# Optimization experiments

Measured on AMD Instinct MI355X. Metric: run time of the kernel, lower is better.

Reference implementation:

```python
import jax, jax.numpy as jnp
import numpy as np

EPS = 1e-5
HEADS = 8


def _bn(x, p):
    # p: [4, C] rows = (gamma, beta, running_mean, running_var); channel axis = 1 (eval-mode BN)
    shape = (1, p.shape[1]) + (1,) * (x.ndim - 2)
    g = p[0].reshape(shape); b = p[1].reshape(shape)
    m = p[2].reshape(shape); v = p[3].reshape(shape)
    return (x - m) * (g / jnp.sqrt(v + EPS)) + b


def _conv1x1(x, w):
    # x: [N, Cin, H, W], w: [Cout, Cin]
    return jnp.einsum('oc,nchw->nohw', w, x)


def _axial(x, kqv_w, kqv_bn, logits_bn, rel_enc, ks, height_dim):
    # x: [B, C, H, W]
    if height_dim:
        x = jnp.transpose(x, (0, 3, 1, 2))  # [B, W, C, H] -> attend over H (=ks)
    else:
        x = jnp.transpose(x, (0, 2, 1, 3))  # [B, H, C, W] -> attend over W (=ks)
    b, w, d, h = x.shape
    dh = d // HEADS
    xf = x.reshape(b * w, d, h)
    kqv = jnp.einsum('oc,ncl->nol', kqv_w, xf)          # conv1d k=1, [n, 2d, h]
    kqv = _bn(kqv, kqv_bn)
    kqv = kqv.reshape(b * w, HEADS, dh * 2, h)
    k = kqv[:, :, : dh // 2]                            # [n, H, dh/2, h]
    q = kqv[:, :, dh // 2: dh]                          # [n, H, dh/2, h]
    v = kqv[:, :, dh:]                                  # [n, H, dh,   h]
    # relative position encodings
    idx = jnp.arange(ks)[None, :] - jnp.arange(ks)[:, None] + ks - 1  # [ks, ks]
    rel = rel_enc[:, idx.reshape(-1)].reshape(dh * 2, ks, ks)
    q_enc = rel[: dh // 2]
    k_enc = rel[dh // 2: dh]
    v_enc = rel[dh:]
    qk = jnp.einsum('nhdx,nhdy->nhxy', q, k)
    qr = jnp.einsum('nhdx,dxy->nhxy', q, q_enc)
    kr = jnp.einsum('nhdx,dxy->nhyx', k, k_enc)         # einsum + transpose(2,3)
    logits = jnp.concatenate([qk, qr, kr], axis=1)       # [n, 3*H, h, h]
    logits = _bn(logits, logits_bn)
    logits = logits.reshape(b * w, 3, HEADS, h, h).sum(axis=1)
    weights = jax.nn.softmax(logits, axis=3)             # [n, H, h, h]
    attn = jnp.einsum('nhxy,nhdy->nhdx', weights, v)
    attn_enc = jnp.einsum('nhxy,dxy->nhdx', weights, v_enc)
    # cat along last dim + reshape + sum(dim=-2) in torch == elementwise sum here
    out = (attn + attn_enc).reshape(b, w, d, h)
    if height_dim:
        out = jnp.transpose(out, (0, 2, 3, 1))  # [B, C, H, W]
    else:
        out = jnp.transpose(out, (0, 2, 1, 3))  # [B, C, H, W]
    return out


def setup_inputs() -> dict:
    key = jax.random.key(0)
    ks = jax.random.split(key, 13)
    def rn(k, shape, s=0.05):
        return jax.random.normal(k, shape, jnp.float32) * s
    def rp(k, shape):
        return jax.random.uniform(k, shape, jnp.float32, minval=0.1, maxval=1.0)
    return {
        'x': jax.random.normal(ks[0], (1, 64, 256, 128), jnp.float32),
        'conv1_w': rn(ks[1], (64, 64)),
        'bn1': rp(ks[2], (4, 64)),
        'kqv_w_h': rn(ks[3], (128, 64)),
        'kqv_bn_h': rp(ks[4], (4, 128)),
        'logits_bn_h': rp(ks[5], (4, 24)),
        'rel_enc_h': rn(ks[6], (16, 511)),
        'kqv_w_w': rn(ks[7], (128, 64)),
        'kqv_bn_w': rp(ks[8], (4, 128)),
        'logits_bn_w': rp(ks[9], (4, 24)),
        'rel_enc_w': rn(ks[10], (16, 255)),
        'conv3_w': rn(ks[11], (64, 64)),
        'bn3': rp(ks[12], (4, 64)),
    }


def reference(x, conv1_w, bn1, kqv_w_h, kqv_bn_h, logits_bn_h, rel_enc_h,
              kqv_w_w, kqv_bn_w, logits_bn_w, rel_enc_w, conv3_w, bn3):
    out = jax.nn.relu(_bn(_conv1x1(x, conv1_w), bn1))
    out = _axial(out, kqv_w_h, kqv_bn_h, logits_bn_h, rel_enc_h, 256, True)
    out = _axial(out, kqv_w_w, kqv_bn_w, logits_bn_w, rel_enc_w, 128, False)
    out = jax.nn.relu(out)
    out = _bn(_conv1x1(out, conv3_w), bn3)
    return jax.nn.relu(out + x)
```

## Files before the change

kernel.cpp:

```cpp
#include <hip/hip_runtime.h>
#include <stdint.h>

#define EPSF 1e-5f
#define LOG2E 1.4426950408889634f

typedef float f32x2 __attribute__((ext_vector_type(2)));
typedef float f32x4 __attribute__((ext_vector_type(4)));

__device__ __forceinline__ float bflo(uint32_t u){ union{uint32_t u;float f;}c; c.u=u<<16; return c.f; }
__device__ __forceinline__ float bfhi(uint32_t u){ union{uint32_t u;float f;}c; c.u=u&0xffff0000u; return c.f; }
__device__ __forceinline__ float bfhiraw(uint32_t u){ union{uint32_t u;float f;}c; c.u=u; return c.f; }
__device__ __forceinline__ uint32_t f2bf(float f){ union{float f;uint32_t u;}c; c.f=f; uint32_t u=c.u; return (u + 0x7fffu + ((u>>16)&1u)) >> 16; }
__device__ __forceinline__ uint32_t pk2(float a, float b){ return f2bf(a) | (f2bf(b)<<16); }

__device__ __forceinline__ f32x2 pk_add(f32x2 a, f32x2 b){
  f32x2 d; asm("v_pk_add_f32 %0, %1, %2" : "=v"(d) : "v"(a), "v"(b)); return d;
}
__device__ __forceinline__ f32x2 pk_mul(f32x2 a, f32x2 b){
  f32x2 d; asm("v_pk_mul_f32 %0, %1, %2" : "=v"(d) : "v"(a), "v"(b)); return d;
}
__device__ __forceinline__ f32x2 pk_fma(f32x2 a, f32x2 b, f32x2 c){
  f32x2 d; asm("v_pk_fma_f32 %0, %1, %2, %3" : "=v"(d) : "v"(a), "v"(b), "v"(c)); return d;
}
__device__ __forceinline__ f32x2 up2(uint32_t u){
  f32x2 r; r.x = bflo(u); r.y = bfhiraw(u); return r;
}

__global__ __launch_bounds__(256)
void k_conv1(const float* __restrict__ in, const float* __restrict__ w,
             const float* __restrict__ bn, float* __restrict__ out,
             const float* __restrict__ relH, const float* __restrict__ relW,
             uint4* __restrict__ rqkH, uint4* __restrict__ rveH,
             uint4* __restrict__ rqkW, uint4* __restrict__ rveW) {
  if (blockIdx.x >= 512) {
    int which = blockIdx.x - 512;
    int NJ = which ? 255 : 511;
    const float* rel = which ? relW : relH;
    uint4* rqk = which ? rqkW : rqkH;
    uint4* rve = which ? rveW : rveH;
    const float* q = rel;
    const float* k = rel + 4*NJ;
    const float* v = rel + 8*NJ;
    for (int j = threadIdx.x; j < NJ; j += 256) {
      int jr = NJ-1-j;
      uint4 a;
      a.x = pk2(q[0*NJ+j], q[1*NJ+j]);
      a.y = pk2(q[2*NJ+j], q[3*NJ+j]);
      a.z = pk2(k[0*NJ+jr], k[1*NJ+jr]);
      a.w = pk2(k[2*NJ+jr], k[3*NJ+jr]);
      rqk[j] = a;
      uint4 b;
      b.x = pk2(v[0*NJ+j], v[1*NJ+j]);
      b.y = pk2(v[2*NJ+j], v[3*NJ+j]);
      b.z = pk2(v[4*NJ+j], v[5*NJ+j]);
      b.w = pk2(v[6*NJ+j], v[7*NJ+j]);
      rve[j] = b;
    }
    return;
  }
  __shared__ float L[64*65];
  int tid = threadIdx.x;
  int p0 = blockIdx.x * 64;
  int lane = tid & 63;
  int wvs = __builtin_amdgcn_readfirstlane(tid >> 6);
  #pragma unroll
  for (int rr = 0; rr < 16; ++rr) {
    int c = wvs*16 + rr;
    L[lane*65 + c] = in[(size_t)c*32768 + p0 + lane];
  }
  __syncthreads();
  f32x2 xv2[32];
  #pragma unroll
  for (int c2 = 0; c2 < 32; ++c2) {
    xv2[c2].x = L[lane*65 + 2*c2];
    xv2[c2].y = L[lane*65 + 2*c2 + 1];
  }
  float val[16];
  #pragma unroll
  for (int r = 0; r < 16; ++r) {
    int o = wvs*16 + r;
    const f32x2* wr = (const f32x2*)(w + o*64);
    f32x2 a2 = {0.f, 0.f};
    #pragma unroll
    for (int c2 = 0; c2 < 32; ++c2) a2 = wr[c2]*xv2[c2] + a2;
    float acc = a2.x + a2.y;
    float s = bn[o] * rsqrtf(bn[192+o] + EPSF);
    val[r] = fmaxf(fmaf(acc, s, fmaf(-bn[128+o], s, bn[64+o])), 0.f);
  }
  __syncthreads();
  #pragma unroll
  for (int r = 0; r < 16; ++r) L[lane*65 + wvs*16 + r] = val[r];
  __syncthreads();
  float4* dst = (float4*)(out + (size_t)p0*64);
  #pragma unroll
  for (int k = 0; k < 4; ++k) {
    int f4 = tid + k*256;
    int f = f4*4; int p = f >> 6, o = f & 63;
    float4 v;
    v.x = L[p*65+o]; v.y = L[p*65+o+1]; v.z = L[p*65+o+2]; v.w = L[p*65+o+3];
    dst[f4] = v;
  }
}

template<int LEN, int RS, int CS>
__global__ __launch_bounds__(512)
void k_kqv(const float* __restrict__ in, const float* __restrict__ w,
           const float* __restrict__ bn, uint4* __restrict__ kvV,
           uint2* __restrict__ kvK, float* __restrict__ qb) {
  __shared__ float L[64*65];
  int tid = threadIdx.x;
  int n = blockIdx.x;
  int y0 = blockIdx.y * 64;
  #pragma unroll
  for (int rr = 0; rr < 8; ++rr) {
    int idx = tid + rr*512;
    int yy = idx >> 6, c = idx & 63;
    L[yy*65 + c] = in[((size_t)(y0+yy)*RS + (size_t)n*CS)*64 + c];
  }
  __syncthreads();
  int hd = __builtin_amdgcn_readfirstlane(tid >> 6);
  int yy = tid & 63;
  f32x2 xv2[32];
  #pragma unroll
  for (int c2 = 0; c2 < 32; ++c2) {
    xv2[c2].x = L[yy*65 + 2*c2];
    xv2[c2].y = L[yy*65 + 2*c2 + 1];
  }
  float val[16];
  #pragma unroll
  for (int r = 0; r < 16; ++r) {
    int o = hd*16 + r;
    const f32x2* wr = (const f32x2*)(w + o*64);
    f32x2 a2 = {0.f, 0.f};
    #pragma unroll
    for (int c2 = 0; c2 < 32; ++c2) a2 = wr[c2]*xv2[c2] + a2;
    float acc = a2.x + a2.y;
    float s = bn[o] * rsqrtf(bn[384+o] + EPSF);
    val[r] = fmaf(acc, s, fmaf(-bn[256+o], s, bn[128+o]));
  }
  size_t base = ((size_t)n*8 + hd)*LEN + (y0 + yy);
  kvK[base] = make_uint2(pk2(val[0],val[1]), pk2(val[2],val[3]));
  kvV[base] = make_uint4(pk2(val[8],val[9]),  pk2(val[10],val[11]),
                         pk2(val[12],val[13]), pk2(val[14],val[15]));
  float4 qq; qq.x = val[4]; qq.y = val[5]; qq.z = val[6]; qq.w = val[7];
  *(float4*)(qb + base*4) = qq;
}

struct E4 { f32x2 qe0, qe1, ke0, ke1; };
struct V4 { f32x2 a, b, c, d; };

__device__ __forceinline__ E4 upQK(uint4 u){
  E4 r; r.qe0 = up2(u.x); r.qe1 = up2(u.y); r.ke0 = up2(u.z); r.ke1 = up2(u.w); return r;
}
__device__ __forceinline__ V4 upVE(uint4 u){
  V4 r; r.a = up2(u.x); r.b = up2(u.y); r.c = up2(u.z); r.d = up2(u.w); return r;
}
__device__ __forceinline__ float pairA(f32x2 q01, f32x2 q23, const E4& e,
                                       f32x2 ktlo, f32x2 kthi) {
  f32x2 t0 = pk_add(q01, e.ke0);
  f32x2 t1 = pk_add(q23, e.ke1);
  f32x2 s  = pk_mul(t0, ktlo);
  s = pk_fma(t1, kthi, s);
  s = pk_fma(q01, e.qe0, s);
  s = pk_fma(q23, e.qe1, s);
  return s.x + s.y;
}
__device__ __forceinline__ void pairB(float ex, const V4& ve,
                                      f32x2 va01, f32x2 va23, f32x2 vb01, f32x2 vb23,
                                      f32x2* A, float& ss) {
  ss += ex;
  f32x2 e2; e2.x = ex; e2.y = ex;
  A[0] = pk_fma(e2, pk_add(va01, ve.a), A[0]);
  A[1] = pk_fma(e2, pk_add(va23, ve.b), A[1]);
  A[2] = pk_fma(e2, pk_add(vb01, ve.c), A[2]);
  A[3] = pk_fma(e2, pk_add(vb23, ve.d), A[3]);
}

template<int LEN, int NB, int G, bool RELUO, int XS, int NS>
__device__ __forceinline__
void attn_body(const uint4* __restrict__ kvV, const uint2* __restrict__ kvK,
               const float* __restrict__ qb, const uint4* __restrict__ rqk,
               const uint4* __restrict__ rve, const float* __restrict__ lbn,
               float* __restrict__ out) {
  constexpr int NJ = 2*LEN-1;
  constexpr int NJ4 = (NJ+1)/4;
  constexpr int XT = LEN/4;
  constexpr int T = NB*XT*G;
  constexpr int YR = LEN/G;
  constexpr size_t S1 = (size_t)NB*LEN*48 + (size_t)NJ4*4*16*2;
  constexpr size_t S2 = (size_t)(G-1)*NB*LEN*40;
  constexpr size_t PS = S1 > S2 ? S1 : S2;
  int nb = blockIdx.x >> 3;
  int hd = blockIdx.x & 7;
  int n0 = nb * NB;
  int t  = threadIdx.x;

  __shared__ __align__(16) char pool[PS];
  f32x4* sKt = (f32x4*)(pool);
  f32x4* sVa = (f32x4*)(pool + (size_t)NB*LEN*16);
  f32x4* sVb = (f32x4*)(pool + (size_t)NB*LEN*32);
  uint4* tQK = (uint4*)(pool + (size_t)NB*LEN*48);
  uint4* tVE = (uint4*)(pool + (size_t)NB*LEN*48 + (size_t)NJ4*64);

  float A0L, A1L, A2L;
  {
    int c0 = hd, c1 = 8+hd, c2 = 16+hd;
    A0L = lbn[c0]*rsqrtf(lbn[72+c0]+EPSF)*LOG2E;
    A1L = lbn[c1]*rsqrtf(lbn[72+c1]+EPSF)*LOG2E;
    A2L = lbn[c2]*rsqrtf(lbn[72+c2]+EPSF)*LOG2E;
  }
  float A0g = (fabsf(A0L) > 1e-25f) ? A0L : copysignf(1e-25f, A0L);
  float ratio = A2L / A0g;

  for (int i = t; i < NB*LEN; i += T) {
    int nn = i / LEN, yy = i % LEN;
    size_t src = ((size_t)(n0+nn)*8 + hd)*LEN + yy;
    uint2 kk = kvK[src];
    uint4 vv = kvV[src];
    f32x4 kt; kt.x=bflo(kk.x)*A0g; kt.y=bfhi(kk.x)*A0g; kt.z=bflo(kk.y)*A0g; kt.w=bfhi(kk.y)*A0g;
    sKt[i] = kt;
    f32x4 va; va.x=bflo(vv.x); va.y=bfhi(vv.x); va.z=bflo(vv.y); va.w=bfhi(vv.y);
    sVa[i] = va;
    f32x4 vb; vb.x=bflo(vv.z); vb.y=bfhi(vv.z); vb.z=bflo(vv.w); vb.w=bfhi(vv.w);
    sVb[i] = vb;
  }
  for (int j = t; j < NJ; j += T) {
    uint4 a = rqk[j];
    uint4 sq;
    sq.x = pk2(bflo(a.x)*A1L,   bfhi(a.x)*A1L);
    sq.y = pk2(bflo(a.y)*A1L,   bfhi(a.y)*A1L);
    sq.z = pk2(bflo(a.z)*ratio, bfhi(a.z)*ratio);
    sq.w = pk2(bflo(a.w)*ratio, bfhi(a.w)*ratio);
    int r = j & 3, mm = j >> 2;
    tQK[r*NJ4 + mm] = sq;
    tVE[r*NJ4 + mm] = rve[j];
  }

  int g  = t / (NB*XT);
  int u  = t % (NB*XT);
  int ni = u / XT;
  int tl = u % XT;
  int y0 = g * YR;
  int x0 = 4 * tl;
  int niL = ni * LEN;
  size_t kb = ((size_t)(n0+ni)*8 + hd)*LEN;

  f32x2 q01[4], q23[4];
  #pragma unroll
  for (int i = 0; i < 4; ++i) {
    f32x4 qq = *(const f32x4*)(qb + (kb + x0 + i)*4);
    q01[i].x = qq.x; q01[i].y = qq.y;
    q23[i].x = qq.z; q23[i].y = qq.w;
  }

  float m[4], ss[4];
  f32x2 acc[4][4];
  #pragma unroll
  for (int i=0;i<4;++i){ m[i]=-3.0e38f; ss[i]=0.f;
    #pragma unroll
    for(int d=0;d<4;++d){ acc[i][d].x=0.f; acc[i][d].y=0.f; } }

  __syncthreads();

  int mi = ((y0 + LEN-1) >> 2) - (x0 >> 2);
  E4 Wq0 = upQK(tQK[0*NJ4 + mi]), Wq1 = upQK(tQK[1*NJ4 + mi]), Wq2 = upQK(tQK[2*NJ4 + mi]);
  V4 Wv0 = upVE(tVE[0*NJ4 + mi]), Wv1 = upVE(tVE[1*NJ4 + mi]), Wv2 = upVE(tVE[2*NJ4 + mi]);

  for (int cc = 0; cc < YR/4; ++cc) {
    int yb = niL + y0 + 4*cc;
    int ma = mi + cc;
    int mb = ma + 1;
    float lr[4][4];
    E4 E3 = upQK(tQK[3*NJ4 + ma]);
    { f32x4 kt = sKt[yb]; f32x2 kl = kt.lo, kh = kt.hi;
      lr[0][0]=pairA(q01[0],q23[0],E3, kl,kh); lr[1][0]=pairA(q01[1],q23[1],Wq2,kl,kh);
      lr[2][0]=pairA(q01[2],q23[2],Wq1,kl,kh); lr[3][0]=pairA(q01[3],q23[3],Wq0,kl,kh); }
    E4 E0 = upQK(tQK[0*NJ4 + mb]);
    { f32x4 kt = sKt[yb+1]; f32x2 kl = kt.lo, kh = kt.hi;
      lr[0][1]=pairA(q01[0],q23[0],E0, kl,kh); lr[1][1]=pairA(q01[1],q23[1],E3, kl,kh);
      lr[2][1]=pairA(q01[2],q23[2],Wq2,kl,kh); lr[3][1]=pairA(q01[3],q23[3],Wq1,kl,kh); }
    E4 E1 = upQK(tQK[1*NJ4 + mb]);
    { f32x4 kt = sKt[yb+2]; f32x2 kl = kt.lo, kh = kt.hi;
      lr[0][2]=pairA(q01[0],q23[0],E1, kl,kh); lr[1][2]=pairA(q01[1],q23[1],E0, kl,kh);
      lr[2][2]=pairA(q01[2],q23[2],E3, kl,kh); lr[3][2]=pairA(q01[3],q23[3],Wq2,kl,kh); }
    E4 E2 = upQK(tQK[2*NJ4 + mb]);
    { f32x4 kt = sKt[yb+3]; f32x2 kl = kt.lo, kh = kt.hi;
      lr[0][3]=pairA(q01[0],q23[0],E2, kl,kh); lr[1][3]=pairA(q01[1],q23[1],E1, kl,kh);
      lr[2][3]=pairA(q01[2],q23[2],E0, kl,kh); lr[3][3]=pairA(q01[3],q23[3],E3, kl,kh); }
    Wq0 = E0; Wq1 = E1; Wq2 = E2;
    float cm[4];
    bool need = false;
    #pragma unroll
    for (int i = 0; i < 4; ++i) {
      cm[i] = fmaxf(fmaxf(lr[i][0], lr[i][1]), fmaxf(lr[i][2], lr[i][3]));
      need = need || (cm[i] > m[i]);
    }
    if (__any(need)) {
      #pragma unroll
      for (int i = 0; i < 4; ++i) {
        float mn = fmaxf(m[i], cm[i]);
        float sc = __builtin_amdgcn_exp2f(m[i] - mn);
        m[i] = mn; ss[i] *= sc;
        f32x2 sc2; sc2.x = sc; sc2.y = sc;
        #pragma unroll
        for (int d = 0; d < 4; ++d) acc[i][d] = pk_mul(acc[i][d], sc2);
      }
    }
    V4 F3 = upVE(tVE[3*NJ4 + ma]);
    { f32x4 va = sVa[yb], vb = sVb[yb];
      pairB(__builtin_amdgcn_exp2f(lr[0][0]-m[0]), F3,  va.lo,va.hi,vb.lo,vb.hi, acc[0], ss[0]);
      pairB(__builtin_amdgcn_exp2f(lr[1][0]-m[1]), Wv2, va.lo,va.hi,vb.lo,vb.hi, acc[1], ss[1]);
      pairB(__builtin_amdgcn_exp2f(lr[2][0]-m[2]), Wv1, va.lo,va.hi,vb.lo,vb.hi, acc[2], ss[2]);
      pairB(__builtin_amdgcn_exp2f(lr[3][0]-m[3]), Wv0, va.lo,va.hi,vb.lo,vb.hi, acc[3], ss[3]); }
    V4 F0 = upVE(tVE[0*NJ4 + mb]);
    { f32x4 va = sVa[yb+1], vb = sVb[yb+1];
      pairB(__builtin_amdgcn_exp2f(lr[0][1]-m[0]), F0,  va.lo,va.hi,vb.lo,vb.hi, acc[0], ss[0]);
      pairB(__builtin_amdgcn_exp2f(lr[1][1]-m[1]), F3,  va.lo,va.hi,vb.lo,vb.hi, acc[1], ss[1]);
      pairB(__builtin_amdgcn_exp2f(lr[2][1]-m[2]), Wv2, va.lo,va.hi,vb.lo,vb.hi, acc[2], ss[2]);
      pairB(__builtin_amdgcn_exp2f(lr[3][1]-m[3]), Wv1, va.lo,va.hi,vb.lo,vb.hi, acc[3], ss[3]); }
    V4 F1 = upVE(tVE[1*NJ4 + mb]);
    { f32x4 va = sVa[yb+2], vb = sVb[yb+2];
      pairB(__builtin_amdgcn_exp2f(lr[0][2]-m[0]), F1,  va.lo,va.hi,vb.lo,vb.hi, acc[0], ss[0]);
      pairB(__builtin_amdgcn_exp2f(lr[1][2]-m[1]), F0,  va.lo,va.hi,vb.lo,vb.hi, acc[1], ss[1]);
      pairB(__builtin_amdgcn_exp2f(lr[2][2]-m[2]), F3,  va.lo,va.hi,vb.lo,vb.hi, acc[2], ss[2]);
      pairB(__builtin_amdgcn_exp2f(lr[3][2]-m[3]), Wv2, va.lo,va.hi,vb.lo,vb.hi, acc[3], ss[3]); }
    V4 F2 = upVE(tVE[2*NJ4 + mb]);
    { f32x4 va = sVa[yb+3], vb = sVb[yb+3];
      pairB(__builtin_amdgcn_exp2f(lr[0][3]-m[0]), F2,  va.lo,va.hi,vb.lo,vb.hi, acc[0], ss[0]);
      pairB(__builtin_amdgcn_exp2f(lr[1][3]-m[1]), F1,  va.lo,va.hi,vb.lo,vb.hi, acc[1], ss[1]);
      pairB(__builtin_amdgcn_exp2f(lr[2][3]-m[2]), F0,  va.lo,va.hi,vb.lo,vb.hi, acc[2], ss[2]);
      pairB(__builtin_amdgcn_exp2f(lr[3][3]-m[3]), F3,  va.lo,va.hi,vb.lo,vb.hi, acc[3], ss[3]); }
    Wv0 = F0; Wv1 = F1; Wv2 = F2;
  }

  __syncthreads();
  float4* M0 = (float4*)(pool);
  float4* M1 = (float4*)(pool + (size_t)(G-1)*NB*LEN*16);
  float2* MS = (float2*)(pool + (size_t)(G-1)*NB*LEN*32);
  int xb = niL + x0;
  if (g > 0) {
    #pragma unroll
    for (int i = 0; i < 4; ++i) {
      int slot = (g-1)*NB*LEN + xb + i;
      M0[slot] = make_float4(acc[i][0].x,acc[i][0].y,acc[i][1].x,acc[i][1].y);
      M1[slot] = make_float4(acc[i][2].x,acc[i][2].y,acc[i][3].x,acc[i][3].y);
      MS[slot] = make_float2(m[i], ss[i]);
    }
  }
  __syncthreads();
  if (g == 0) {
    #pragma unroll
    for (int i = 0; i < 4; ++i) {
      float M = m[i];
      float2 oms[G-1];
      #pragma unroll
      for (int gg = 1; gg < G; ++gg) {
        oms[gg-1] = MS[(gg-1)*NB*LEN + xb + i];
        M = fmaxf(M, oms[gg-1].x);
      }
      float w0 = __builtin_amdgcn_exp2f(m[i] - M);
      float st = ss[i]*w0;
      float a[8];
      a[0]=acc[i][0].x*w0; a[1]=acc[i][0].y*w0; a[2]=acc[i][1].x*w0; a[3]=acc[i][1].y*w0;
      a[4]=acc[i][2].x*w0; a[5]=acc[i][2].y*w0; a[6]=acc[i][3].x*w0; a[7]=acc[i][3].y*w0;
      #pragma unroll
      for (int gg = 1; gg < G; ++gg) {
        int slot = (gg-1)*NB*LEN + xb + i;
        float wg = __builtin_amdgcn_exp2f(oms[gg-1].x - M);
        st += oms[gg-1].y*wg;
        float4 a0 = M0[slot];
        float4 a1 = M1[slot];
        a[0] = fmaf(a0.x, wg, a[0]); a[1] = fmaf(a0.y, wg, a[1]);
        a[2] = fmaf(a0.z, wg, a[2]); a[3] = fmaf(a0.w, wg, a[3]);
        a[4] = fmaf(a1.x, wg, a[4]); a[5] = fmaf(a1.y, wg, a[5]);
        a[6] = fmaf(a1.z, wg, a[6]); a[7] = fmaf(a1.w, wg, a[7]);
      }
      float inv = 1.0f / st;
      float* dst = out + ((size_t)(x0+i)*XS + (size_t)(n0+ni)*NS)*64 + hd*8;
      float4 lo, hi;
      lo.x = a[0]*inv; lo.y = a[1]*inv; lo.z = a[2]*inv; lo.w = a[3]*inv;
      hi.x = a[4]*inv; hi.y = a[5]*inv; hi.z = a[6]*inv; hi.w = a[7]*inv;
      if (RELUO) {
        lo.x=fmaxf(lo.x,0.f); lo.y=fmaxf(lo.y,0.f); lo.z=fmaxf(lo.z,0.f); lo.w=fmaxf(lo.w,0.f);
        hi.x=fmaxf(hi.x,0.f); hi.y=fmaxf(hi.y,0.f); hi.z=fmaxf(hi.z,0.f); hi.w=fmaxf(hi.w,0.f);
      }
      *(float4*)dst = lo;
      *((float4*)dst + 1) = hi;
    }
  }
}

__global__ __launch_bounds__(256, 2)
void k_attnH(const uint4* __restrict__ kvV, const uint2* __restrict__ kvK,
             const float* __restrict__ qb, const uint4* __restrict__ rqk,
             const uint4* __restrict__ rve, const float* __restrict__ lbn,
             float* __restrict__ out) {
  attn_body<256,1,4,false,128,1>(kvV, kvK, qb, rqk, rve, lbn, out);
}
__global__ __launch_bounds__(256, 2)
void k_attnW(const uint4* __restrict__ kvV, const uint2* __restrict__ kvK,
             const float* __restrict__ qb, const uint4* __restrict__ rqk,
             const uint4* __restrict__ rve, const float* __restrict__ lbn,
             float* __restrict__ out) {
  attn_body<128,2,4,true,1,128>(kvV, kvK, qb, rqk, rve, lbn, out);
}

__global__ __launch_bounds__(256)
void k_conv3(const float* __restrict__ in, const float* __restrict__ w,
             const float* __restrict__ bn, const float* __restrict__ resid,
             float* __restrict__ out) {
  __shared__ float L[64*65];
  int tid = threadIdx.x;
  int p0 = blockIdx.x * 64;
  const float4* src = (const float4*)(in + (size_t)p0*64);
  #pragma unroll
  for (int k = 0; k < 4; ++k) {
    int f4 = tid + k*256;
    float4 v = src[f4];
    int f = f4*4; int p = f >> 6, o = f & 63;
    L[p*65+o] = v.x; L[p*65+o+1] = v.y; L[p*65+o+2] = v.z; L[p*65+o+3] = v.w;
  }
  __syncthreads();
  int lane = tid & 63;
  int wvs = __builtin_amdgcn_readfirstlane(tid >> 6);
  f32x2 xv2[32];
  #pragma unroll
  for (int c2 = 0; c2 < 32; ++c2) {
    xv2[c2].x = L[lane*65 + 2*c2];
    xv2[c2].y = L[lane*65 + 2*c2 + 1];
  }
  #pragma unroll
  for (int r = 0; r < 16; ++r) {
    int o = wvs*16 + r;
    const f32x2* wr = (const f32x2*)(w + o*64);
    f32x2 a2 = {0.f, 0.f};
    #pragma unroll
    for (int c2 = 0; c2 < 32; ++c2) a2 = wr[c2]*xv2[c2] + a2;
    float acc = a2.x + a2.y;
    float s = bn[o] * rsqrtf(bn[192+o] + EPSF);
    float val = fmaf(acc, s, fmaf(-bn[128+o], s, bn[64+o]));
    size_t idx = (size_t)o*32768 + p0 + lane;
    out[idx] = fmaxf(val + resid[idx], 0.f);
  }
}

extern "C" void kernel_launch(void* const* d_in, const int* in_sizes, int n_in,
                              void* d_out, int out_size, void* d_ws, size_t ws_size,
                              hipStream_t stream) {
  const float* x         = (const float*)d_in[0];
  const float* conv1_w   = (const float*)d_in[1];
  const float* bn1       = (const float*)d_in[2];
  const float* kqv_w_h   = (const float*)d_in[3];
  const float* kqv_bn_h  = (const float*)d_in[4];
  const float* lbn_h     = (const float*)d_in[5];
  const float* rel_h     = (const float*)d_in[6];
  const float* kqv_w_w   = (const float*)d_in[7];
  const float* kqv_bn_w  = (const float*)d_in[8];
  const float* lbn_w     = (const float*)d_in[9];
  const float* rel_w     = (const float*)d_in[10];
  const float* conv3_w   = (const float*)d_in[11];
  const float* bn3       = (const float*)d_in[12];
  float* outp = (float*)d_out;
  char* ws = (char*)d_ws;

  float* A    = (float*)(ws);
  uint4* kvV  = (uint4*)(ws + 8388608);
  uint2* kvK  = (uint2*)(ws + 12582912);
  float* qb   = (float*)(ws + 14680064);
  uint4* rqkH = (uint4*)(ws + 18874368);
  uint4* rveH = (uint4*)(ws + 18882560);
  uint4* rqkW = (uint4*)(ws + 18890752);
  uint4* rveW = (uint4*)(ws + 18894848);

  k_conv1<<<514, 256, 0, stream>>>(x, conv1_w, bn1, A,
                                   rel_h, rel_w, rqkH, rveH, rqkW, rveW);

  k_kqv<256,128,1><<<dim3(128,4), 512, 0, stream>>>(A, kqv_w_h, kqv_bn_h, kvV, kvK, qb);
  k_attnH<<<1024, 256, 0, stream>>>(kvV, kvK, qb, rqkH, rveH, lbn_h, A);

  k_kqv<128,1,128><<<dim3(256,2), 512, 0, stream>>>(A, kqv_w_w, kqv_bn_w, kvV, kvK, qb);
  k_attnW<<<1024, 256, 0, stream>>>(kvV, kvK, qb, rqkW, rveW, lbn_w, A);

  k_conv3<<<512, 256, 0, stream>>>(A, conv3_w, bn3, x, outp);
}
```

Before: 171.5 us.

## Switch attention operands from bf16 to fp16 with packed dot2 and half-width LDS

Intermediate K, V and relative-encoding tables are now stored as fp16 instead of bf16. The attention inner loop computes logits with fdot2 on packed halves and adds V to V-encodings with packed fp16 adds, instead of unpacking to fp32 and using v_pk_fma. K and V now stay packed in shared memory, which halves that LDS footprint and the load traffic. The aim is fewer ALU instructions per logit and per accumulation, traded for fp16 range and rounding risk and more scalar fp16-to-fp32 converts in the PV accumulation.

```diff
diff --git a/kernel.cpp b/kernel.cpp
--- a/kernel.cpp
+++ b/kernel.cpp
@@ -6,25 +6,26 @@
 
 typedef float f32x2 __attribute__((ext_vector_type(2)));
 typedef float f32x4 __attribute__((ext_vector_type(4)));
-
-__device__ __forceinline__ float bflo(uint32_t u){ union{uint32_t u;float f;}c; c.u=u<<16; return c.f; }
-__device__ __forceinline__ float bfhi(uint32_t u){ union{uint32_t u;float f;}c; c.u=u&0xffff0000u; return c.f; }
-__device__ __forceinline__ float bfhiraw(uint32_t u){ union{uint32_t u;float f;}c; c.u=u; return c.f; }
-__device__ __forceinline__ uint32_t f2bf(float f){ union{float f;uint32_t u;}c; c.f=f; uint32_t u=c.u; return (u + 0x7fffu + ((u>>16)&1u)) >> 16; }
-__device__ __forceinline__ uint32_t pk2(float a, float b){ return f2bf(a) | (f2bf(b)<<16); }
-
-__device__ __forceinline__ f32x2 pk_add(f32x2 a, f32x2 b){
-  f32x2 d; asm("v_pk_add_f32 %0, %1, %2" : "=v"(d) : "v"(a), "v"(b)); return d;
-}
-__device__ __forceinline__ f32x2 pk_mul(f32x2 a, f32x2 b){
-  f32x2 d; asm("v_pk_mul_f32 %0, %1, %2" : "=v"(d) : "v"(a), "v"(b)); return d;
-}
-__device__ __forceinline__ f32x2 pk_fma(f32x2 a, f32x2 b, f32x2 c){
-  f32x2 d; asm("v_pk_fma_f32 %0, %1, %2, %3" : "=v"(d) : "v"(a), "v"(b), "v"(c)); return d;
-}
-__device__ __forceinline__ f32x2 up2(uint32_t u){
-  f32x2 r; r.x = bflo(u); r.y = bfhiraw(u); return r;
-}
+typedef _Float16 h2 __attribute__((ext_vector_type(2)));
+union UH2 { uint32_t u; h2 h; };
+
+__device__ __forceinline__ uint32_t pkh(float a, float b){
+  UH2 c; c.h.x = (_Float16)a; c.h.y = (_Float16)b; return c.u;
+}
+__device__ __forceinline__ h2 ash2(uint32_t u){ UH2 c; c.u = u; return c.h; }
+__device__ __forceinline__ uint32_t padd16(uint32_t a, uint32_t b){
+  UH2 c; c.h = ash2(a) + ash2(b); return c.u;
+}
+#if __has_builtin(__builtin_amdgcn_fdot2)
+__device__ __forceinline__ float fdot2u(uint32_t a, uint32_t b, float c){
+  return __builtin_amdgcn_fdot2(ash2(a), ash2(b), c, false);
+}
+#else
+__device__ __forceinline__ float fdot2u(uint32_t a, uint32_t b, float c){
+  h2 x = ash2(a), y = ash2(b);
+  return fmaf((float)x.y, (float)y.y, fmaf((float)x.x, (float)y.x, c));
+}
+#endif
 
 __global__ __launch_bounds__(256)
 void k_conv1(const float* __restrict__ in, const float* __restrict__ w,
@@ -44,16 +45,16 @@
     for (int j = threadIdx.x; j < NJ; j += 256) {
       int jr = NJ-1-j;
       uint4 a;
-      a.x = pk2(q[0*NJ+j], q[1*NJ+j]);
-      a.y = pk2(q[2*NJ+j], q[3*NJ+j]);
-      a.z = pk2(k[0*NJ+jr], k[1*NJ+jr]);
-      a.w = pk2(k[2*NJ+jr], k[3*NJ+jr]);
+      a.x = pkh(q[0*NJ+j], q[1*NJ+j]);
+      a.y = pkh(q[2*NJ+j], q[3*NJ+j]);
+      a.z = pkh(k[0*NJ+jr], k[1*NJ+jr]);
+      a.w = pkh(k[2*NJ+jr], k[3*NJ+jr]);
       rqk[j] = a;
       uint4 b;
-      b.x = pk2(v[0*NJ+j], v[1*NJ+j]);
-      b.y = pk2(v[2*NJ+j], v[3*NJ+j]);
-      b.z = pk2(v[4*NJ+j], v[5*NJ+j]);
-      b.w = pk2(v[6*NJ+j], v[7*NJ+j]);
+      b.x = pkh(v[0*NJ+j], v[1*NJ+j]);
+      b.y = pkh(v[2*NJ+j], v[3*NJ+j]);
+      b.z = pkh(v[4*NJ+j], v[5*NJ+j]);
+      b.w = pkh(v[6*NJ+j], v[7*NJ+j]);
       rve[j] = b;
     }
     return;
@@ -139,41 +140,34 @@
     val[r] = fmaf(acc, s, fmaf(-bn[256+o], s, bn[128+o]));
   }
   size_t base = ((size_t)n*8 + hd)*LEN + (y0 + yy);
-  kvK[base] = make_uint2(pk2(val[0],val[1]), pk2(val[2],val[3]));
-  kvV[base] = make_uint4(pk2(val[8],val[9]),  pk2(val[10],val[11]),
-                         pk2(val[12],val[13]), pk2(val[14],val[15]));
+  kvK[base] = make_uint2(pkh(val[0],val[1]), pkh(val[2],val[3]));
+  kvV[base] = make_uint4(pkh(val[8],val[9]),  pkh(val[10],val[11]),
+                         pkh(val[12],val[13]), pkh(val[14],val[15]));
   float4 qq; qq.x = val[4]; qq.y = val[5]; qq.z = val[6]; qq.w = val[7];
   *(float4*)(qb + base*4) = qq;
 }
 
-struct E4 { f32x2 qe0, qe1, ke0, ke1; };
-struct V4 { f32x2 a, b, c, d; };
-
-__device__ __forceinline__ E4 upQK(uint4 u){
-  E4 r; r.qe0 = up2(u.x); r.qe1 = up2(u.y); r.ke0 = up2(u.z); r.ke1 = up2(u.w); return r;
-}
-__device__ __forceinline__ V4 upVE(uint4 u){
-  V4 r; r.a = up2(u.x); r.b = up2(u.y); r.c = up2(u.z); r.d = up2(u.w); return r;
-}
-__device__ __forceinline__ float pairA(f32x2 q01, f32x2 q23, const E4& e,
-                                       f32x2 ktlo, f32x2 kthi) {
-  f32x2 t0 = pk_add(q01, e.ke0);
-  f32x2 t1 = pk_add(q23, e.ke1);
-  f32x2 s  = pk_mul(t0, ktlo);
-  s = pk_fma(t1, kthi, s);
-  s = pk_fma(q01, e.qe0, s);
-  s = pk_fma(q23, e.qe1, s);
-  return s.x + s.y;
-}
-__device__ __forceinline__ void pairB(float ex, const V4& ve,
-                                      f32x2 va01, f32x2 va23, f32x2 vb01, f32x2 vb23,
-                                      f32x2* A, float& ss) {
-  ss += ex;
-  f32x2 e2; e2.x = ex; e2.y = ex;
-  A[0] = pk_fma(e2, pk_add(va01, ve.a), A[0]);
-  A[1] = pk_fma(e2, pk_add(va23, ve.b), A[1]);
-  A[2] = pk_fma(e2, pk_add(vb01, ve.c), A[2]);
-  A[3] = pk_fma(e2, pk_add(vb23, ve.d), A[3]);
+__device__ __forceinline__ float pairA(uint32_t q01, uint32_t q23, uint4 e,
+                                       uint32_t kt01, uint32_t kt23) {
+  uint32_t t01 = padd16(q01, e.z);
+  uint32_t t23 = padd16(q23, e.w);
+  return fdot2u(kt01, t01, fdot2u(kt23, t23, fdot2u(q01, e.x, fdot2u(q23, e.y, 0.f))));
+}
+__device__ __forceinline__ void pairB(float e, uint4 ve, uint4 vv,
+                                      float* A, float& ss) {
+  ss += e;
+  h2 w0 = ash2(vv.x) + ash2(ve.x);
+  h2 w1 = ash2(vv.y) + ash2(ve.y);
+  h2 w2 = ash2(vv.z) + ash2(ve.z);
+  h2 w3 = ash2(vv.w) + ash2(ve.w);
+  A[0] = fmaf((float)w0.x, e, A[0]);
+  A[1] = fmaf((float)w0.y, e, A[1]);
+  A[2] = fmaf((float)w1.x, e, A[2]);
+  A[3] = fmaf((float)w1.y, e, A[3]);
+  A[4] = fmaf((float)w2.x, e, A[4]);
+  A[5] = fmaf((float)w2.y, e, A[5]);
+  A[6] = fmaf((float)w3.x, e, A[6]);
+  A[7] = fmaf((float)w3.y, e, A[7]);
 }
 
 template<int LEN, int NB, int G, bool RELUO, int XS, int NS>
@@ -187,7 +181,7 @@
   constexpr int XT = LEN/4;
   constexpr int T = NB*XT*G;
   constexpr int YR = LEN/G;
-  constexpr size_t S1 = (size_t)NB*LEN*48 + (size_t)NJ4*4*16*2;
+  constexpr size_t S1 = (size_t)NB*LEN*24 + (size_t)NJ4*4*16*2;
   constexpr size_t S2 = (size_t)(G-1)*NB*LEN*40;
   constexpr size_t PS = S1 > S2 ? S1 : S2;
   int nb = blockIdx.x >> 3;
@@ -196,11 +190,10 @@
   int t  = threadIdx.x;
 
   __shared__ __align__(16) char pool[PS];
-  f32x4* sKt = (f32x4*)(pool);
-  f32x4* sVa = (f32x4*)(pool + (size_t)NB*LEN*16);
-  f32x4* sVb = (f32x4*)(pool + (size_t)NB*LEN*32);
-  uint4* tQK = (uint4*)(pool + (size_t)NB*LEN*48);
-  uint4* tVE = (uint4*)(pool + (size_t)NB*LEN*48 + (size_t)NJ4*64);
+  uint2* sKt = (uint2*)(pool);
+  uint4* sV2 = (uint4*)(pool + (size_t)NB*LEN*8);
+  uint4* tQK = (uint4*)(pool + (size_t)NB*LEN*24);
+  uint4* tVE = (uint4*)(pool + (size_t)NB*LEN*24 + (size_t)NJ4*64);
 
   float A0L, A1L, A2L;
   {
@@ -216,21 +209,19 @@
     int nn = i / LEN, yy = i % LEN;
     size_t src = ((size_t)(n0+nn)*8 + hd)*LEN + yy;
     uint2 kk = kvK[src];
-    uint4 vv = kvV[src];
-    f32x4 kt; kt.x=bflo(kk.x)*A0g; kt.y=bfhi(kk.x)*A0g; kt.z=bflo(kk.y)*A0g; kt.w=bfhi(kk.y)*A0g;
-    sKt[i] = kt;
-    f32x4 va; va.x=bflo(vv.x); va.y=bfhi(vv.x); va.z=bflo(vv.y); va.w=bfhi(vv.y);
-    sVa[i] = va;
-    f32x4 vb; vb.x=bflo(vv.z); vb.y=bfhi(vv.z); vb.z=bflo(vv.w); vb.w=bfhi(vv.w);
-    sVb[i] = vb;
+    h2 a = ash2(kk.x), b = ash2(kk.y);
+    sKt[i] = make_uint2(pkh(A0g*(float)a.x, A0g*(float)a.y),
+                        pkh(A0g*(float)b.x, A0g*(float)b.y));
+    sV2[i] = kvV[src];
   }
   for (int j = t; j < NJ; j += T) {
     uint4 a = rqk[j];
+    h2 q01 = ash2(a.x), q23 = ash2(a.y), k01 = ash2(a.z), k23 = ash2(a.w);
     uint4 sq;
-    sq.x = pk2(bflo(a.x)*A1L,   bfhi(a.x)*A1L);
-    sq.y = pk2(bflo(a.y)*A1L,   bfhi(a.y)*A1L);
-    sq.z = pk2(bflo(a.z)*ratio, bfhi(a.z)*ratio);
-    sq.w = pk2(bflo(a.w)*ratio, bfhi(a.w)*ratio);
+    sq.x = pkh(A1L*(float)q01.x,   A1L*(float)q01.y);
+    sq.y = pkh(A1L*(float)q23.x,   A1L*(float)q23.y);
+    sq.z = pkh(ratio*(float)k01.x, ratio*(float)k01.y);
+    sq.w = pkh(ratio*(float)k23.x, ratio*(float)k23.y);
     int r = j & 3, mm = j >> 2;
     tQK[r*NJ4 + mm] = sq;
     tVE[r*NJ4 + mm] = rve[j];
@@ -245,48 +236,47 @@
   int niL = ni * LEN;
   size_t kb = ((size_t)(n0+ni)*8 + hd)*LEN;
 
-  f32x2 q01[4], q23[4];
+  uint32_t q01[4], q23[4];
   #pragma unroll
   for (int i = 0; i < 4; ++i) {
     f32x4 qq = *(const f32x4*)(qb + (kb + x0 + i)*4);
-    q01[i].x = qq.x; q01[i].y = qq.y;
-    q23[i].x = qq.z; q23[i].y = qq.w;
-  }
-
-  float m[4], ss[4];
-  f32x2 acc[4][4];
+    q01[i] = pkh(qq.x, qq.y);
+    q23[i] = pkh(qq.z, qq.w);
+  }
+
+  float m[4], ss[4], acc[4][8];
   #pragma unroll
   for (int i=0;i<4;++i){ m[i]=-3.0e38f; ss[i]=0.f;
     #pragma unroll
-    for(int d=0;d<4;++d){ acc[i][d].x=0.f; acc[i][d].y=0.f; } }
+    for(int d=0;d<8;++d) acc[i][d]=0.f; }
 
   __syncthreads();
 
   int mi = ((y0 + LEN-1) >> 2) - (x0 >> 2);
-  E4 Wq0 = upQK(tQK[0*NJ4 + mi]), Wq1 = upQK(tQK[1*NJ4 + mi]), Wq2 = upQK(tQK[2*NJ4 + mi]);
-  V4 Wv0 = upVE(tVE[0*NJ4 + mi]), Wv1 = upVE(tVE[1*NJ4 + mi]), Wv2 = upVE(tVE[2*NJ4 + mi]);
+  uint4 Wq0 = tQK[0*NJ4 + mi], Wq1 = tQK[1*NJ4 + mi], Wq2 = tQK[2*NJ4 + mi];
+  uint4 Wv0 = tVE[0*NJ4 + mi], Wv1 = tVE[1*NJ4 + mi], Wv2 = tVE[2*NJ4 + mi];
 
   for (int cc = 0; cc < YR/4; ++cc) {
     int yb = niL + y0 + 4*cc;
     int ma = mi + cc;
     int mb = ma + 1;
     float lr[4][4];
-    E4 E3 = upQK(tQK[3*NJ4 + ma]);
-    { f32x4 kt = sKt[yb]; f32x2 kl = kt.lo, kh = kt.hi;
-      lr[0][0]=pairA(q01[0],q23[0],E3, kl,kh); lr[1][0]=pairA(q01[1],q23[1],Wq2,kl,kh);
-      lr[2][0]=pairA(q01[2],q23[2],Wq1,kl,kh); lr[3][0]=pairA(q01[3],q23[3],Wq0,kl,kh); }
-    E4 E0 = upQK(tQK[0*NJ4 + mb]);
-    { f32x4 kt = sKt[yb+1]; f32x2 kl = kt.lo, kh = kt.hi;
-      lr[0][1]=pairA(q01[0],q23[0],E0, kl,kh); lr[1][1]=pairA(q01[1],q23[1],E3, kl,kh);
-      lr[2][1]=pairA(q01[2],q23[2],Wq2,kl,kh); lr[3][1]=pairA(q01[3],q23[3],Wq1,kl,kh); }
-    E4 E1 = upQK(tQK[1*NJ4 + mb]);
-    { f32x4 kt = sKt[yb+2]; f32x2 kl = kt.lo, kh = kt.hi;
-      lr[0][2]=pairA(q01[0],q23[0],E1, kl,kh); lr[1][2]=pairA(q01[1],q23[1],E0, kl,kh);
-      lr[2][2]=pairA(q01[2],q23[2],E3, kl,kh); lr[3][2]=pairA(q01[3],q23[3],Wq2,kl,kh); }
-    E4 E2 = upQK(tQK[2*NJ4 + mb]);
-    { f32x4 kt = sKt[yb+3]; f32x2 kl = kt.lo, kh = kt.hi;
-      lr[0][3]=pairA(q01[0],q23[0],E2, kl,kh); lr[1][3]=pairA(q01[1],q23[1],E1, kl,kh);
-      lr[2][3]=pairA(q01[2],q23[2],E0, kl,kh); lr[3][3]=pairA(q01[3],q23[3],E3, kl,kh); }
+    uint4 E3 = tQK[3*NJ4 + ma];
+    { uint2 kt = sKt[yb];
+      lr[0][0]=pairA(q01[0],q23[0],E3, kt.x,kt.y); lr[1][0]=pairA(q01[1],q23[1],Wq2,kt.x,kt.y);
+      lr[2][0]=pairA(q01[2],q23[2],Wq1,kt.x,kt.y); lr[3][0]=pairA(q01[3],q23[3],Wq0,kt.x,kt.y); }
+    uint4 E0 = tQK[0*NJ4 + mb];
+    { uint2 kt = sKt[yb+1];
+      lr[0][1]=pairA(q01[0],q23[0],E0, kt.x,kt.y); lr[1][1]=pairA(q01[1],q23[1],E3, kt.x,kt.y);
+      lr[2][1]=pairA(q01[2],q23[2],Wq2,kt.x,kt.y); lr[3][1]=pairA(q01[3],q23[3],Wq1,kt.x,kt.y); }
+    uint4 E1 = tQK[1*NJ4 + mb];
+    { uint2 kt = sKt[yb+2];
+      lr[0][2]=pairA(q01[0],q23[0],E1, kt.x,kt.y); lr[1][2]=pairA(q01[1],q23[1],E0, kt.x,kt.y);
+      lr[2][2]=pairA(q01[2],q23[2],E3, kt.x,kt.y); lr[3][2]=pairA(q01[3],q23[3],Wq2,kt.x,kt.y); }
+    uint4 E2 = tQK[2*NJ4 + mb];
+    { uint2 kt = sKt[yb+3];
+      lr[0][3]=pairA(q01[0],q23[0],E2, kt.x,kt.y); lr[1][3]=pairA(q01[1],q23[1],E1, kt.x,kt.y);
+      lr[2][3]=pairA(q01[2],q23[2],E0, kt.x,kt.y); lr[3][3]=pairA(q01[3],q23[3],E3, kt.x,kt.y); }
     Wq0 = E0; Wq1 = E1; Wq2 = E2;
     float cm[4];
     bool need = false;
@@ -301,35 +291,34 @@
         float mn = fmaxf(m[i], cm[i]);
         float sc = __builtin_amdgcn_exp2f(m[i] - mn);
         m[i] = mn; ss[i] *= sc;
-        f32x2 sc2; sc2.x = sc; sc2.y = sc;
         #pragma unroll
-        for (int d = 0; d < 4; ++d) acc[i][d] = pk_mul(acc[i][d], sc2);
+        for (int d = 0; d < 8; ++d) acc[i][d] *= sc;
       }
     }
-    V4 F3 = upVE(tVE[3*NJ4 + ma]);
-    { f32x4 va = sVa[yb], vb = sVb[yb];
-      pairB(__builtin_amdgcn_exp2f(lr[0][0]-m[0]), F3,  va.lo,va.hi,vb.lo,vb.hi, acc[0], ss[0]);
-      pairB(__builtin_amdgcn_exp2f(lr[1][0]-m[1]), Wv2, va.lo,va.hi,vb.lo,vb.hi, acc[1], ss[1]);
-      pairB(__builtin_amdgcn_exp2f(lr[2][0]-m[2]), Wv1, va.lo,va.hi,vb.lo,vb.hi, acc[2], ss[2]);
-      pairB(__builtin_amdgcn_exp2f(lr[3][0]-m[3]), Wv0, va.lo,va.hi,vb.lo,vb.hi, acc[3], ss[3]); }
-    V4 F0 = upVE(tVE[0*NJ4 + mb]);
-    { f32x4 va = sVa[yb+1], vb = sVb[yb+1];
-      pairB(__builtin_amdgcn_exp2f(lr[0][1]-m[0]), F0,  va.lo,va.hi,vb.lo,vb.hi, acc[0], ss[0]);
-      pairB(__builtin_amdgcn_exp2f(lr[1][1]-m[1]), F3,  va.lo,va.hi,vb.lo,vb.hi, acc[1], ss[1]);
-      pairB(__builtin_amdgcn_exp2f(lr[2][1]-m[2]), Wv2, va.lo,va.hi,vb.lo,vb.hi, acc[2], ss[2]);
-      pairB(__builtin_amdgcn_exp2f(lr[3][1]-m[3]), Wv1, va.lo,va.hi,vb.lo,vb.hi, acc[3], ss[3]); }
-    V4 F1 = upVE(tVE[1*NJ4 + mb]);
-    { f32x4 va = sVa[yb+2], vb = sVb[yb+2];
-      pairB(__builtin_amdgcn_exp2f(lr[0][2]-m[0]), F1,  va.lo,va.hi,vb.lo,vb.hi, acc[0], ss[0]);
-      pairB(__builtin_amdgcn_exp2f(lr[1][2]-m[1]), F0,  va.lo,va.hi,vb.lo,vb.hi, acc[1], ss[1]);
-      pairB(__builtin_amdgcn_exp2f(lr[2][2]-m[2]), F3,  va.lo,va.hi,vb.lo,vb.hi, acc[2], ss[2]);
-      pairB(__builtin_amdgcn_exp2f(lr[3][2]-m[3]), Wv2, va.lo,va.hi,vb.lo,vb.hi, acc[3], ss[3]); }
-    V4 F2 = upVE(tVE[2*NJ4 + mb]);
-    { f32x4 va = sVa[yb+3], vb = sVb[yb+3];
-      pairB(__builtin_amdgcn_exp2f(lr[0][3]-m[0]), F2,  va.lo,va.hi,vb.lo,vb.hi, acc[0], ss[0]);
-      pairB(__builtin_amdgcn_exp2f(lr[1][3]-m[1]), F1,  va.lo,va.hi,vb.lo,vb.hi, acc[1], ss[1]);
-      pairB(__builtin_amdgcn_exp2f(lr[2][3]-m[2]), F0,  va.lo,va.hi,vb.lo,vb.hi, acc[2], ss[2]);
-      pairB(__builtin_amdgcn_exp2f(lr[3][3]-m[3]), F3,  va.lo,va.hi,vb.lo,vb.hi, acc[3], ss[3]); }
+    uint4 F3 = tVE[3*NJ4 + ma];
+    { uint4 vv = sV2[yb];
+      pairB(__builtin_amdgcn_exp2f(lr[0][0]-m[0]), F3,  vv, acc[0], ss[0]);
+      pairB(__builtin_amdgcn_exp2f(lr[1][0]-m[1]), Wv2, vv, acc[1], ss[1]);
+      pairB(__builtin_amdgcn_exp2f(lr[2][0]-m[2]), Wv1, vv, acc[2], ss[2]);
+      pairB(__builtin_amdgcn_exp2f(lr[3][0]-m[3]), Wv0, vv, acc[3], ss[3]); }
+    uint4 F0 = tVE[0*NJ4 + mb];
+    { uint4 vv = sV2[yb+1];
+      pairB(__builtin_amdgcn_exp2f(lr[0][1]-m[0]), F0,  vv, acc[0], ss[0]);
+      pairB(__builtin_amdgcn_exp2f(lr[1][1]-m[1]), F3,  vv, acc[1], ss[1]);
+      pairB(__builtin_amdgcn_exp2f(lr[2][1]-m[2]), Wv2, vv, acc[2], ss[2]);
+      pairB(__builtin_amdgcn_exp2f(lr[3][1]-m[3]), Wv1, vv, acc[3], ss[3]); }
+    uint4 F1 = tVE[1*NJ4 + mb];
+    { uint4 vv = sV2[yb+2];
+      pairB(__builtin_amdgcn_exp2f(lr[0][2]-m[0]), F1,  vv, acc[0], ss[0]);
+      pairB(__builtin_amdgcn_exp2f(lr[1][2]-m[1]), F0,  vv, acc[1], ss[1]);
+      pairB(__builtin_amdgcn_exp2f(lr[2][2]-m[2]), F3,  vv, acc[2], ss[2]);
+      pairB(__builtin_amdgcn_exp2f(lr[3][2]-m[3]), Wv2, vv, acc[3], ss[3]); }
+    uint4 F2 = tVE[2*NJ4 + mb];
+    { uint4 vv = sV2[yb+3];
+      pairB(__builtin_amdgcn_exp2f(lr[0][3]-m[0]), F2,  vv, acc[0], ss[0]);
+      pairB(__builtin_amdgcn_exp2f(lr[1][3]-m[1]), F1,  vv, acc[1], ss[1]);
+      pairB(__builtin_amdgcn_exp2f(lr[2][3]-m[2]), F0,  vv, acc[2], ss[2]);
+      pairB(__builtin_amdgcn_exp2f(lr[3][3]-m[3]), F3,  vv, acc[3], ss[3]); }
     Wv0 = F0; Wv1 = F1; Wv2 = F2;
   }
 
@@ -342,8 +331,8 @@
     #pragma unroll
     for (int i = 0; i < 4; ++i) {
       int slot = (g-1)*NB*LEN + xb + i;
-      M0[slot] = make_float4(acc[i][0].x,acc[i][0].y,acc[i][1].x,acc[i][1].y);
-      M1[slot] = make_float4(acc[i][2].x,acc[i][2].y,acc[i][3].x,acc[i][3].y);
+      M0[slot] = make_float4(acc[i][0],acc[i][1],acc[i][2],acc[i][3]);
+      M1[slot] = make_float4(acc[i][4],acc[i][5],acc[i][6],acc[i][7]);
       MS[slot] = make_float2(m[i], ss[i]);
     }
   }
@@ -361,8 +350,8 @@
       float w0 = __builtin_amdgcn_exp2f(m[i] - M);
       float st = ss[i]*w0;
       float a[8];
-      a[0]=acc[i][0].x*w0; a[1]=acc[i][0].y*w0; a[2]=acc[i][1].x*w0; a[3]=acc[i][1].y*w0;
-      a[4]=acc[i][2].x*w0; a[5]=acc[i][2].y*w0; a[6]=acc[i][3].x*w0; a[7]=acc[i][3].y*w0;
+      #pragma unroll
+      for (int d = 0; d < 8; ++d) a[d] = acc[i][d]*w0;
       #pragma unroll
       for (int gg = 1; gg < G; ++gg) {
         int slot = (gg-1)*NB*LEN + xb + i;
```

After: 177.5 us. +3.5%, slower.

## Fuse kqv projection into axial attention kernels, computing per-head projections in-block

Applied to the files above, without the earlier changes.

Removes the separate kqv projection kernels and computes each head's k, q and v projection inside the attention block from the staged input rows. This eliminates the bf16 kqv/q intermediate buffers in global memory and two kernel launches, and it keeps the projection values in fp32. In exchange, each of the 8 head blocks re-reads the same input rows, multiplying input traffic, and shared memory usage grows. Attention output now ping-pongs between two workspace buffers.

```diff
diff --git a/kernel.cpp b/kernel.cpp
--- a/kernel.cpp
+++ b/kernel.cpp
@@ -102,50 +102,6 @@
   }
 }
 
-template<int LEN, int RS, int CS>
-__global__ __launch_bounds__(512)
-void k_kqv(const float* __restrict__ in, const float* __restrict__ w,
-           const float* __restrict__ bn, uint4* __restrict__ kvV,
-           uint2* __restrict__ kvK, float* __restrict__ qb) {
-  __shared__ float L[64*65];
-  int tid = threadIdx.x;
-  int n = blockIdx.x;
-  int y0 = blockIdx.y * 64;
-  #pragma unroll
-  for (int rr = 0; rr < 8; ++rr) {
-    int idx = tid + rr*512;
-    int yy = idx >> 6, c = idx & 63;
-    L[yy*65 + c] = in[((size_t)(y0+yy)*RS + (size_t)n*CS)*64 + c];
-  }
-  __syncthreads();
-  int hd = __builtin_amdgcn_readfirstlane(tid >> 6);
-  int yy = tid & 63;
-  f32x2 xv2[32];
-  #pragma unroll
-  for (int c2 = 0; c2 < 32; ++c2) {
-    xv2[c2].x = L[yy*65 + 2*c2];
-    xv2[c2].y = L[yy*65 + 2*c2 + 1];
-  }
-  float val[16];
-  #pragma unroll
-  for (int r = 0; r < 16; ++r) {
-    int o = hd*16 + r;
-    const f32x2* wr = (const f32x2*)(w + o*64);
-    f32x2 a2 = {0.f, 0.f};
-    #pragma unroll
-    for (int c2 = 0; c2 < 32; ++c2) a2 = wr[c2]*xv2[c2] + a2;
-    float acc = a2.x + a2.y;
-    float s = bn[o] * rsqrtf(bn[384+o] + EPSF);
-    val[r] = fmaf(acc, s, fmaf(-bn[256+o], s, bn[128+o]));
-  }
-  size_t base = ((size_t)n*8 + hd)*LEN + (y0 + yy);
-  kvK[base] = make_uint2(pk2(val[0],val[1]), pk2(val[2],val[3]));
-  kvV[base] = make_uint4(pk2(val[8],val[9]),  pk2(val[10],val[11]),
-                         pk2(val[12],val[13]), pk2(val[14],val[15]));
-  float4 qq; qq.x = val[4]; qq.y = val[5]; qq.z = val[6]; qq.w = val[7];
-  *(float4*)(qb + base*4) = qq;
-}
-
 struct E4 { f32x2 qe0, qe1, ke0, ke1; };
 struct V4 { f32x2 a, b, c, d; };
 
@@ -176,10 +132,10 @@
   A[3] = pk_fma(e2, pk_add(vb23, ve.d), A[3]);
 }
 
-template<int LEN, int NB, int G, bool RELUO, int XS, int NS>
+template<int LEN, int NB, int G, bool RELUO, int XS, int NS, int RS, int CS>
 __device__ __forceinline__
-void attn_body(const uint4* __restrict__ kvV, const uint2* __restrict__ kvK,
-               const float* __restrict__ qb, const uint4* __restrict__ rqk,
+void attn_body(const float* __restrict__ in, const float* __restrict__ kw,
+               const float* __restrict__ kbn, const uint4* __restrict__ rqk,
                const uint4* __restrict__ rve, const float* __restrict__ lbn,
                float* __restrict__ out) {
   constexpr int NJ = 2*LEN-1;
@@ -187,9 +143,8 @@
   constexpr int XT = LEN/4;
   constexpr int T = NB*XT*G;
   constexpr int YR = LEN/G;
-  constexpr size_t S1 = (size_t)NB*LEN*48 + (size_t)NJ4*4*16*2;
-  constexpr size_t S2 = (size_t)(G-1)*NB*LEN*40;
-  constexpr size_t PS = S1 > S2 ? S1 : S2;
+  static_assert(T == 256, "chunk staging assumes 256 threads");
+  constexpr size_t PS = (size_t)NB*LEN*64 + (size_t)NJ4*128 + (size_t)64*65*4;
   int nb = blockIdx.x >> 3;
   int hd = blockIdx.x & 7;
   int n0 = nb * NB;
@@ -201,6 +156,8 @@
   f32x4* sVb = (f32x4*)(pool + (size_t)NB*LEN*32);
   uint4* tQK = (uint4*)(pool + (size_t)NB*LEN*48);
   uint4* tVE = (uint4*)(pool + (size_t)NB*LEN*48 + (size_t)NJ4*64);
+  f32x4* tQf = (f32x4*)(pool + (size_t)NB*LEN*48 + (size_t)NJ4*128);
+  float* Lb  = (float*)(pool + (size_t)NB*LEN*64 + (size_t)NJ4*128);
 
   float A0L, A1L, A2L;
   {
@@ -212,18 +169,6 @@
   float A0g = (fabsf(A0L) > 1e-25f) ? A0L : copysignf(1e-25f, A0L);
   float ratio = A2L / A0g;
 
-  for (int i = t; i < NB*LEN; i += T) {
-    int nn = i / LEN, yy = i % LEN;
-    size_t src = ((size_t)(n0+nn)*8 + hd)*LEN + yy;
-    uint2 kk = kvK[src];
-    uint4 vv = kvV[src];
-    f32x4 kt; kt.x=bflo(kk.x)*A0g; kt.y=bfhi(kk.x)*A0g; kt.z=bflo(kk.y)*A0g; kt.w=bfhi(kk.y)*A0g;
-    sKt[i] = kt;
-    f32x4 va; va.x=bflo(vv.x); va.y=bfhi(vv.x); va.z=bflo(vv.y); va.w=bfhi(vv.y);
-    sVa[i] = va;
-    f32x4 vb; vb.x=bflo(vv.z); vb.y=bfhi(vv.z); vb.z=bflo(vv.w); vb.w=bfhi(vv.w);
-    sVb[i] = vb;
-  }
   for (int j = t; j < NJ; j += T) {
     uint4 a = rqk[j];
     uint4 sq;
@@ -236,6 +181,58 @@
     tVE[r*NJ4 + mm] = rve[j];
   }
 
+  int lane = t & 63;
+  int wv = __builtin_amdgcn_readfirstlane(t >> 6);
+  float sC[4], bC[4];
+  #pragma unroll
+  for (int r = 0; r < 4; ++r) {
+    int o = hd*16 + wv*4 + r;
+    float s = kbn[o] * rsqrtf(kbn[384+o] + EPSF);
+    sC[r] = s;
+    bC[r] = fmaf(-kbn[256+o], s, kbn[128+o]);
+  }
+  for (int c0 = 0; c0 < NB*LEN; c0 += 64) {
+    __syncthreads();
+    #pragma unroll
+    for (int k = 0; k < 16; ++k) {
+      int idx = t + k*256;
+      int row = idx >> 6, c = idx & 63;
+      int gi = c0 + row;
+      int nn = gi / LEN, yy = gi % LEN;
+      Lb[row*65 + c] = in[((size_t)yy*RS + (size_t)(n0+nn)*CS)*64 + c];
+    }
+    __syncthreads();
+    f32x2 xv2[32];
+    #pragma unroll
+    for (int c2 = 0; c2 < 32; ++c2) {
+      xv2[c2].x = Lb[lane*65 + 2*c2];
+      xv2[c2].y = Lb[lane*65 + 2*c2 + 1];
+    }
+    float val[4];
+    #pragma unroll
+    for (int r = 0; r < 4; ++r) {
+      int o = hd*16 + wv*4 + r;
+      const f32x2* wr = (const f32x2*)(kw + o*64);
+      f32x2 a2 = {0.f, 0.f};
+      #pragma unroll
+      for (int c2 = 0; c2 < 32; ++c2) a2 = wr[c2]*xv2[c2] + a2;
+      val[r] = fmaf(a2.x + a2.y, sC[r], bC[r]);
+    }
+    int i = c0 + lane;
+    f32x4 v4; v4.x = val[0]; v4.y = val[1]; v4.z = val[2]; v4.w = val[3];
+    if (wv == 0) {
+      f32x4 kt; kt.x = val[0]*A0g; kt.y = val[1]*A0g; kt.z = val[2]*A0g; kt.w = val[3]*A0g;
+      sKt[i] = kt;
+    } else if (wv == 1) {
+      tQf[i] = v4;
+    } else if (wv == 2) {
+      sVa[i] = v4;
+    } else {
+      sVb[i] = v4;
+    }
+  }
+  __syncthreads();
+
   int g  = t / (NB*XT);
   int u  = t % (NB*XT);
   int ni = u / XT;
@@ -243,12 +240,11 @@
   int y0 = g * YR;
   int x0 = 4 * tl;
   int niL = ni * LEN;
-  size_t kb = ((size_t)(n0+ni)*8 + hd)*LEN;
 
   f32x2 q01[4], q23[4];
   #pragma unroll
   for (int i = 0; i < 4; ++i) {
-    f32x4 qq = *(const f32x4*)(qb + (kb + x0 + i)*4);
+    f32x4 qq = tQf[niL + x0 + i];
     q01[i].x = qq.x; q01[i].y = qq.y;
     q23[i].x = qq.z; q23[i].y = qq.w;
   }
@@ -259,8 +255,6 @@
   for (int i=0;i<4;++i){ m[i]=-3.0e38f; ss[i]=0.f;
     #pragma unroll
     for(int d=0;d<4;++d){ acc[i][d].x=0.f; acc[i][d].y=0.f; } }
-
-  __syncthreads();
 
   int mi = ((y0 + LEN-1) >> 2) - (x0 >> 2);
   E4 Wq0 = upQK(tQK[0*NJ4 + mi]), Wq1 = upQK(tQK[1*NJ4 + mi]), Wq2 = upQK(tQK[2*NJ4 + mi]);
@@ -391,18 +385,18 @@
 }
 
 __global__ __launch_bounds__(256, 2)
-void k_attnH(const uint4* __restrict__ kvV, const uint2* __restrict__ kvK,
-             const float* __restrict__ qb, const uint4* __restrict__ rqk,
+void k_attnH(const float* __restrict__ in, const float* __restrict__ kw,
+             const float* __restrict__ kbn, const uint4* __restrict__ rqk,
              const uint4* __restrict__ rve, const float* __restrict__ lbn,
              float* __restrict__ out) {
-  attn_body<256,1,4,false,128,1>(kvV, kvK, qb, rqk, rve, lbn, out);
+  attn_body<256,1,4,false,128,1,128,1>(in, kw, kbn, rqk, rve, lbn, out);
 }
 __global__ __launch_bounds__(256, 2)
-void k_attnW(const uint4* __restrict__ kvV, const uint2* __restrict__ kvK,
-             const float* __restrict__ qb, const uint4* __restrict__ rqk,
+void k_attnW(const float* __restrict__ in, const float* __restrict__ kw,
+             const float* __restrict__ kbn, const uint4* __restrict__ rqk,
              const uint4* __restrict__ rve, const float* __restrict__ lbn,
              float* __restrict__ out) {
-  attn_body<128,2,4,true,1,128>(kvV, kvK, qb, rqk, rve, lbn, out);
+  attn_body<128,2,4,true,1,128,1,128>(in, kw, kbn, rqk, rve, lbn, out);
 }
 
 __global__ __launch_bounds__(256)
@@ -464,22 +458,18 @@
   char* ws = (char*)d_ws;
 
   float* A    = (float*)(ws);
-  uint4* kvV  = (uint4*)(ws + 8388608);
-  uint2* kvK  = (uint2*)(ws + 12582912);
-  float* qb   = (float*)(ws + 14680064);
-  uint4* rqkH = (uint4*)(ws + 18874368);
-  uint4* rveH = (uint4*)(ws + 18882560);
-  uint4* rqkW = (uint4*)(ws + 18890752);
-  uint4* rveW = (uint4*)(ws + 18894848);
+  float* B    = (float*)(ws + 8388608);
+  uint4* rqkH = (uint4*)(ws + 16777216);
+  uint4* rveH = (uint4*)(ws + 16785408);
+  uint4* rqkW = (uint4*)(ws + 16793600);
+  uint4* rveW = (uint4*)(ws + 16797696);
 
   k_conv1<<<514, 256, 0, stream>>>(x, conv1_w, bn1, A,
                                    rel_h, rel_w, rqkH, rveH, rqkW, rveW);
 
-  k_kqv<256,128,1><<<dim3(128,4), 512, 0, stream>>>(A, kqv_w_h, kqv_bn_h, kvV, kvK, qb);
-  k_attnH<<<1024, 256, 0, stream>>>(kvV, kvK, qb, rqkH, rveH, lbn_h, A);
-
-  k_kqv<128,1,128><<<dim3(256,2), 512, 0, stream>>>(A, kqv_w_w, kqv_bn_w, kvV, kvK, qb);
-  k_attnW<<<1024, 256, 0, stream>>>(kvV, kvK, qb, rqkW, rveW, lbn_w, A);
+  k_attnH<<<1024, 256, 0, stream>>>(A, kqv_w_h, kqv_bn_h, rqkH, rveH, lbn_h, B);
+
+  k_attnW<<<1024, 256, 0, stream>>>(B, kqv_w_w, kqv_bn_w, rqkW, rveW, lbn_w, A);
 
   k_conv3<<<512, 256, 0, stream>>>(A, conv3_w, bn3, x, outp);
 }
```

Result: slower. 176.9 us (+3.1%).
